# Performance work log

Measured on AMD Instinct MI355X. Metric: run time of the kernel, lower is better.

Reference implementation:

```python
import jax, jax.numpy as jnp
import numpy as np

N_NODES = 100000
N_EDGES = 1000000
H = 128  # hidden_size


def setup_inputs() -> dict:
    key = jax.random.key(0)
    ks = jax.random.split(key, 8)
    emb = jax.random.normal(ks[0], (N_NODES, H), dtype=jnp.float32)
    edge_index = jax.random.randint(ks[1], (2, N_EDGES), 0, N_NODES, dtype=jnp.int64)
    # MLP([2H, 4H, H, 1]) weights (Kaiming-ish scaled normals)
    W1 = jax.random.normal(ks[2], (2 * H, 4 * H), dtype=jnp.float32) / np.sqrt(2 * H).astype(np.float32)
    b1 = jnp.zeros((4 * H,), dtype=jnp.float32)
    W2 = jax.random.normal(ks[3], (4 * H, H), dtype=jnp.float32) / np.sqrt(4 * H).astype(np.float32)
    b2 = jnp.zeros((H,), dtype=jnp.float32)
    W3 = jax.random.normal(ks[4], (H, 1), dtype=jnp.float32) / np.sqrt(H).astype(np.float32)
    b3 = jnp.zeros((1,), dtype=jnp.float32)
    return {"emb": emb, "edge_index": edge_index,
            "W1": W1, "b1": b1, "W2": W2, "b2": b2, "W3": W3, "b3": b3}


def reference(emb, edge_index, W1, b1, W2, b2, W3, b3):
    # ExtractorMLP.forward with learn_edge_att=True, eval mode.
    col = edge_index[0]
    row = edge_index[1]
    # edge-gather + concat: [E, 2H]
    f12 = jnp.concatenate([emb[col], emb[row]], axis=-1)
    # MLP([2H, 4H, H, 1]); Dropout is identity in eval mode
    h = jax.nn.relu(f12 @ W1 + b1)          # [E, 4H]
    h = jax.nn.relu(h @ W2 + b2)            # [E, H]
    att_log_logits = h @ W3 + b3            # [E, 1]
    # concrete_sample with training=False -> plain sigmoid
    att = jax.nn.sigmoid(att_log_logits)
    return att
```

## Files before the change

kernel.cpp:

```cpp
#include <hip/hip_runtime.h>
#include <math.h>

#define E_TOTAL   1000000
#define HDIM      128
#define K1        256
#define N1        512
#define N2        128
#define M_TILE    64
#define BLOCK     512

typedef _Float16 f16;
typedef _Float16 f16_4 __attribute__((ext_vector_type(4)));
typedef _Float16 f16_8 __attribute__((ext_vector_type(8)));
typedef float    f32_4 __attribute__((ext_vector_type(4)));

__global__ void prep_kernel(const float* __restrict__ W1, const float* __restrict__ W2,
                            f16* __restrict__ W1F, f16* __restrict__ W2F) {
    int t = blockIdx.x * blockDim.x + threadIdx.x;
    const int total1 = K1 * N1;
    const int total2 = N1 * N2;
    if (t < total1) {
        int v    = t & 7;
        int lane = (t >> 3) & 63;
        int ks   = (t >> 9) & 7;
        int tile = t >> 12;
        int n = tile * 16 + (lane & 15);
        int k = ks * 32 + (lane >> 4) * 8 + v;
        W1F[t] = (f16)W1[k * N1 + n];
    } else if (t < total1 + total2) {
        int u = t - total1;
        int v    = u & 7;
        int lane = (u >> 3) & 63;
        int kc   = (u >> 9) & 15;
        int tile = u >> 13;
        int n = tile * 16 + (lane & 15);
        int k = kc * 32 + (lane >> 4) * 8 + v;
        W2F[u] = (f16)W2[k * N2 + n];
    }
}

__global__ __launch_bounds__(BLOCK, 4) void edge_mlp_kernel(
    const float* __restrict__ emb,
    const int*   __restrict__ eidx,
    const f16*   __restrict__ W1F,
    const float* __restrict__ b1,
    const f16*   __restrict__ W2F,
    const float* __restrict__ b2,
    const float* __restrict__ W3,
    const float* __restrict__ b3,
    float* __restrict__ out)
{
    __shared__ __align__(16) f16 sA[M_TILE * 256];
    __shared__ __align__(16) f16 sH1[M_TILE * 256];
    f16* sH2 = sA;

    const int tid = threadIdx.x;
    const int e0  = blockIdx.x * M_TILE;

    {
        const int m    = tid >> 3;
        const int side = (tid >> 2) & 1;
        const int sub  = tid & 3;
        const int node = eidx[side * E_TOTAL + e0 + m];
        const float4* src = (const float4*)(emb + (size_t)node * HDIM);
        #pragma unroll
        for (int i = 0; i < 8; ++i) {
            const int c4 = sub + 4 * i;
            float4 f = src[c4];
            f16_4 v = { (f16)f.x, (f16)f.y, (f16)f.z, (f16)f.w };
            const int ch  = side * 16 + (c4 >> 1);
            const int off = (c4 & 1) * 4;
            *(f16_4*)(sA + m * 256 + (((ch ^ (m & 7)) << 3) + off)) = v;
        }
    }
    __syncthreads();

    const int wv   = tid >> 6;
    const int lane = tid & 63;
    const int lrow = lane & 15;
    const int quad = lane >> 4;

    f32_4 acc2[4];
    #pragma unroll
    for (int et = 0; et < 4; ++et) acc2[et] = (f32_4){0.f, 0.f, 0.f, 0.f};

    #pragma unroll
    for (int h = 0; h < 2; ++h) {
        {
            f32_4 acc1[2][4];
            #pragma unroll
            for (int wnt = 0; wnt < 2; ++wnt)
                #pragma unroll
                for (int et = 0; et < 4; ++et) acc1[wnt][et] = (f32_4){0.f, 0.f, 0.f, 0.f};

            #pragma unroll
            for (int ks = 0; ks < 8; ++ks) {
                const int c = ks * 4 + quad;
                f16_8 ef[4];
                #pragma unroll
                for (int et = 0; et < 4; ++et) {
                    const int row = et * 16 + lrow;
                    ef[et] = *(const f16_8*)(sA + row * 256 + ((c ^ (row & 7)) << 3));
                }
                #pragma unroll
                for (int wnt = 0; wnt < 2; ++wnt) {
                    const int tile = h * 16 + wv * 2 + wnt;
                    f16_8 wf = *(const f16_8*)(W1F + (((tile * 8 + ks) * 64 + lane) << 3));
                    #pragma unroll
                    for (int et = 0; et < 4; ++et)
                        acc1[wnt][et] = __builtin_amdgcn_mfma_f32_16x16x32_f16(wf, ef[et], acc1[wnt][et], 0, 0, 0);
                }
            }
            #pragma unroll
            for (int wnt = 0; wnt < 2; ++wnt) {
                const float4 bias = *(const float4*)(b1 + h * 256 + wv * 32 + wnt * 16 + quad * 4);
                const int klocal = wv * 32 + wnt * 16 + quad * 4;
                const int ch  = klocal >> 3;
                const int off = klocal & 7;
                #pragma unroll
                for (int et = 0; et < 4; ++et) {
                    const int row = et * 16 + lrow;
                    f16_4 hv;
                    #pragma unroll
                    for (int i = 0; i < 4; ++i) {
                        float v = acc1[wnt][et][i] + ((const float*)&bias)[i];
                        hv[i] = (f16)(v > 0.f ? v : 0.f);
                    }
                    *(f16_4*)(sH1 + row * 256 + (((ch ^ (row & 7)) << 3) + off)) = hv;
                }
            }
        }
        __syncthreads();

        #pragma unroll
        for (int ks = 0; ks < 8; ++ks) {
            const int c = ks * 4 + quad;
            f16_8 ef[4];
            #pragma unroll
            for (int et = 0; et < 4; ++et) {
                const int row = et * 16 + lrow;
                ef[et] = *(const f16_8*)(sH1 + row * 256 + ((c ^ (row & 7)) << 3));
            }
            f16_8 wf = *(const f16_8*)(W2F + (((wv * 16 + h * 8 + ks) * 64 + lane) << 3));
            #pragma unroll
            for (int et = 0; et < 4; ++et)
                acc2[et] = __builtin_amdgcn_mfma_f32_16x16x32_f16(wf, ef[et], acc2[et], 0, 0, 0);
        }
        __syncthreads();
    }

    {
        const float4 b2v = *(const float4*)(b2 + wv * 16 + quad * 4);
        const int wn  = wv * 16 + quad * 4;
        const int ch  = wn >> 3;
        const int off = wn & 7;
        #pragma unroll
        for (int et = 0; et < 4; ++et) {
            const int row = et * 16 + lrow;
            f16_4 hv;
            #pragma unroll
            for (int i = 0; i < 4; ++i) {
                float v = acc2[et][i] + ((const float*)&b2v)[i];
                hv[i] = (f16)(v > 0.f ? v : 0.f);
            }
            *(f16_4*)(sH2 + row * 128 + (((ch ^ (row & 7)) << 3) + off)) = hv;
        }
    }
    __syncthreads();

    {
        const int m = tid >> 3;
        const int j = tid & 7;
        const int c0 = (2 * j)     ^ (m & 7);
        const int c1 = (2 * j + 1) ^ (m & 7);
        f16_8 a = *(const f16_8*)(sH2 + m * 128 + (c0 << 3));
        f16_8 b = *(const f16_8*)(sH2 + m * 128 + (c1 << 3));
        const float* w3p = W3 + j * 16;
        float s = 0.f;
        #pragma unroll
        for (int t = 0; t < 8; ++t) s += (float)a[t] * w3p[t];
        #pragma unroll
        for (int t = 0; t < 8; ++t) s += (float)b[t] * w3p[8 + t];
        s += __shfl_xor(s, 1);
        s += __shfl_xor(s, 2);
        s += __shfl_xor(s, 4);
        if (j == 0) {
            const float logit = s + b3[0];
            out[e0 + m] = 1.0f / (1.0f + __expf(-logit));
        }
    }
}

extern "C" void kernel_launch(void* const* d_in, const int* in_sizes, int n_in,
                              void* d_out, int out_size, void* d_ws, size_t ws_size,
                              hipStream_t stream) {
    const float* emb  = (const float*)d_in[0];
    const int*   eidx = (const int*)d_in[1];
    const float* W1   = (const float*)d_in[2];
    const float* b1   = (const float*)d_in[3];
    const float* W2   = (const float*)d_in[4];
    const float* b2   = (const float*)d_in[5];
    const float* W3   = (const float*)d_in[6];
    const float* b3   = (const float*)d_in[7];
    float* out = (float*)d_out;

    f16* W1F = (f16*)d_ws;
    f16* W2F = W1F + K1 * N1;

    const int prep_total = K1 * N1 + N1 * N2;
    prep_kernel<<<(prep_total + 255) / 256, 256, 0, stream>>>(W1, W2, W1F, W2F);

    edge_mlp_kernel<<<E_TOTAL / M_TILE, BLOCK, 0, stream>>>(
        emb, eidx, W1F, b1, W2F, b2, W3, b3, out);
}
```

Baseline: 688.4 us.

## Switch to 32x32x16 MFMA tiles and pre-convert embeddings to fp16

Replaces the 16x16x32 MFMA layout with 32x32x16 tiles. Each wave now owns one 32-row edge tile and two 32-column weight tiles, which cuts LDS A-fragment reads per MFMA, and both weight pre-pack layouts are rewritten to match. When the workspace is large enough, a separate pass converts the node embedding table to fp16, so the edge gather reads half the bytes per row. The cost is an extra conversion kernel (about 51 MB read, 26 MB written) and a workspace-size-dependent code path.

```diff
diff --git a/kernel.cpp b/kernel.cpp
--- a/kernel.cpp
+++ b/kernel.cpp
@@ -10,37 +10,46 @@
 #define BLOCK     512
 
 typedef _Float16 f16;
-typedef _Float16 f16_4 __attribute__((ext_vector_type(4)));
-typedef _Float16 f16_8 __attribute__((ext_vector_type(8)));
-typedef float    f32_4 __attribute__((ext_vector_type(4)));
-
-__global__ void prep_kernel(const float* __restrict__ W1, const float* __restrict__ W2,
-                            f16* __restrict__ W1F, f16* __restrict__ W2F) {
+typedef _Float16 f16_4  __attribute__((ext_vector_type(4)));
+typedef _Float16 f16_8  __attribute__((ext_vector_type(8)));
+typedef float    f32_16 __attribute__((ext_vector_type(16)));
+
+__global__ void prep_weights(const float* __restrict__ W1, const float* __restrict__ W2,
+                             f16* __restrict__ W1F, f16* __restrict__ W2F) {
     int t = blockIdx.x * blockDim.x + threadIdx.x;
     const int total1 = K1 * N1;
     const int total2 = N1 * N2;
     if (t < total1) {
         int v    = t & 7;
         int lane = (t >> 3) & 63;
-        int ks   = (t >> 9) & 7;
-        int tile = t >> 12;
-        int n = tile * 16 + (lane & 15);
-        int k = ks * 32 + (lane >> 4) * 8 + v;
+        int kc   = (t >> 9) & 15;
+        int nt   = t >> 13;
+        int k = kc * 16 + (lane >> 5) * 8 + v;
+        int n = nt * 32 + (lane & 31);
         W1F[t] = (f16)W1[k * N1 + n];
     } else if (t < total1 + total2) {
         int u = t - total1;
         int v    = u & 7;
         int lane = (u >> 3) & 63;
-        int kc   = (u >> 9) & 15;
-        int tile = u >> 13;
-        int n = tile * 16 + (lane & 15);
-        int k = kc * 32 + (lane >> 4) * 8 + v;
+        int kcg  = (u >> 9) & 31;
+        int nt   = u >> 14;
+        int k = kcg * 16 + (lane >> 5) * 8 + v;
+        int n = nt * 32 + (lane & 31);
         W2F[u] = (f16)W2[k * N2 + n];
     }
 }
 
+__global__ void prep_emb(const float* __restrict__ emb, f16* __restrict__ emb16) {
+    int t = blockIdx.x * blockDim.x + threadIdx.x;
+    float4 f = ((const float4*)emb)[t];
+    f16_4 v = { (f16)f.x, (f16)f.y, (f16)f.z, (f16)f.w };
+    ((f16_4*)emb16)[t] = v;
+}
+
+template <bool F16EMB>
 __global__ __launch_bounds__(BLOCK, 4) void edge_mlp_kernel(
     const float* __restrict__ emb,
+    const f16*   __restrict__ emb16,
     const int*   __restrict__ eidx,
     const f16*   __restrict__ W1F,
     const float* __restrict__ b1,
@@ -57,7 +66,20 @@
     const int tid = threadIdx.x;
     const int e0  = blockIdx.x * M_TILE;
 
-    {
+    if (F16EMB) {
+        const int row  = tid >> 2;
+        const int g    = tid & 3;
+        const int m    = row >> 1;
+        const int side = row & 1;
+        const int node = eidx[side * E_TOTAL + e0 + m];
+        const f16_8* src = (const f16_8*)(emb16 + (size_t)node * HDIM + g * 32);
+        #pragma unroll
+        for (int i = 0; i < 4; ++i) {
+            f16_8 v = src[i];
+            const int ch = side * 16 + g * 4 + i;
+            *(f16_8*)(sA + m * 256 + ((ch ^ (m & 7)) << 3)) = v;
+        }
+    } else {
         const int m    = tid >> 3;
         const int side = (tid >> 2) & 1;
         const int sub  = tid & 3;
@@ -77,93 +99,79 @@
 
     const int wv   = tid >> 6;
     const int lane = tid & 63;
-    const int lrow = lane & 15;
-    const int quad = lane >> 4;
-
-    f32_4 acc2[4];
+    const int l31  = lane & 31;
+    const int lh   = lane >> 5;
+    const int et   = wv & 1;
+    const int ntg  = wv >> 1;
+    const int arow = et * 32 + l31;
+    const int asw  = arow & 7;
+
+    f32_16 acc2 = {0.f};
+
     #pragma unroll
-    for (int et = 0; et < 4; ++et) acc2[et] = (f32_4){0.f, 0.f, 0.f, 0.f};
-
-    #pragma unroll
-    for (int h = 0; h < 2; ++h) {
+    for (int hh = 0; hh < 2; ++hh) {
         {
-            f32_4 acc1[2][4];
-            #pragma unroll
-            for (int wnt = 0; wnt < 2; ++wnt)
+            f32_16 acc1[2] = {{0.f}, {0.f}};
+            #pragma unroll
+            for (int kc = 0; kc < 16; ++kc) {
+                const int ch = kc * 2 + lh;
+                f16_8 ef = *(const f16_8*)(sA + arow * 256 + ((ch ^ asw) << 3));
                 #pragma unroll
-                for (int et = 0; et < 4; ++et) acc1[wnt][et] = (f32_4){0.f, 0.f, 0.f, 0.f};
-
-            #pragma unroll
-            for (int ks = 0; ks < 8; ++ks) {
-                const int c = ks * 4 + quad;
-                f16_8 ef[4];
+                for (int j = 0; j < 2; ++j) {
+                    const int nt = hh * 8 + ntg * 2 + j;
+                    f16_8 wf = *(const f16_8*)(W1F + (((nt * 16 + kc) * 64 + lane) << 3));
+                    acc1[j] = __builtin_amdgcn_mfma_f32_32x32x16_f16(wf, ef, acc1[j], 0, 0, 0);
+                }
+            }
+            #pragma unroll
+            for (int j = 0; j < 2; ++j) {
+                const int nth = ntg * 2 + j;
                 #pragma unroll
-                for (int et = 0; et < 4; ++et) {
-                    const int row = et * 16 + lrow;
-                    ef[et] = *(const f16_8*)(sA + row * 256 + ((c ^ (row & 7)) << 3));
-                }
-                #pragma unroll
-                for (int wnt = 0; wnt < 2; ++wnt) {
-                    const int tile = h * 16 + wv * 2 + wnt;
-                    f16_8 wf = *(const f16_8*)(W1F + (((tile * 8 + ks) * 64 + lane) << 3));
-                    #pragma unroll
-                    for (int et = 0; et < 4; ++et)
-                        acc1[wnt][et] = __builtin_amdgcn_mfma_f32_16x16x32_f16(wf, ef[et], acc1[wnt][et], 0, 0, 0);
-                }
-            }
-            #pragma unroll
-            for (int wnt = 0; wnt < 2; ++wnt) {
-                const float4 bias = *(const float4*)(b1 + h * 256 + wv * 32 + wnt * 16 + quad * 4);
-                const int klocal = wv * 32 + wnt * 16 + quad * 4;
-                const int ch  = klocal >> 3;
-                const int off = klocal & 7;
-                #pragma unroll
-                for (int et = 0; et < 4; ++et) {
-                    const int row = et * 16 + lrow;
+                for (int g = 0; g < 4; ++g) {
+                    const int wnh = nth * 32 + lh * 4 + g * 8;
+                    const float4 bv = *(const float4*)(b1 + hh * 256 + wnh);
                     f16_4 hv;
                     #pragma unroll
                     for (int i = 0; i < 4; ++i) {
-                        float v = acc1[wnt][et][i] + ((const float*)&bias)[i];
+                        float v = acc1[j][g * 4 + i] + ((const float*)&bv)[i];
                         hv[i] = (f16)(v > 0.f ? v : 0.f);
                     }
-                    *(f16_4*)(sH1 + row * 256 + (((ch ^ (row & 7)) << 3) + off)) = hv;
+                    const int ch  = wnh >> 3;
+                    const int off = wnh & 7;
+                    *(f16_4*)(sH1 + arow * 256 + (((ch ^ asw) << 3) + off)) = hv;
                 }
             }
         }
         __syncthreads();
 
+        {
+            const int nt2 = ntg;
+            #pragma unroll
+            for (int kc = 0; kc < 16; ++kc) {
+                const int ch = kc * 2 + lh;
+                f16_8 ef = *(const f16_8*)(sH1 + arow * 256 + ((ch ^ asw) << 3));
+                f16_8 wf = *(const f16_8*)(W2F + (((nt2 * 32 + hh * 16 + kc) * 64 + lane) << 3));
+                acc2 = __builtin_amdgcn_mfma_f32_32x32x16_f16(wf, ef, acc2, 0, 0, 0);
+            }
+        }
+        __syncthreads();
+    }
+
+    {
+        const int nt2 = ntg;
         #pragma unroll
-        for (int ks = 0; ks < 8; ++ks) {
-            const int c = ks * 4 + quad;
-            f16_8 ef[4];
-            #pragma unroll
-            for (int et = 0; et < 4; ++et) {
-                const int row = et * 16 + lrow;
-                ef[et] = *(const f16_8*)(sH1 + row * 256 + ((c ^ (row & 7)) << 3));
-            }
-            f16_8 wf = *(const f16_8*)(W2F + (((wv * 16 + h * 8 + ks) * 64 + lane) << 3));
-            #pragma unroll
-            for (int et = 0; et < 4; ++et)
-                acc2[et] = __builtin_amdgcn_mfma_f32_16x16x32_f16(wf, ef[et], acc2[et], 0, 0, 0);
-        }
-        __syncthreads();
-    }
-
-    {
-        const float4 b2v = *(const float4*)(b2 + wv * 16 + quad * 4);
-        const int wn  = wv * 16 + quad * 4;
-        const int ch  = wn >> 3;
-        const int off = wn & 7;
-        #pragma unroll
-        for (int et = 0; et < 4; ++et) {
-            const int row = et * 16 + lrow;
+        for (int g = 0; g < 4; ++g) {
+            const int wn = nt2 * 32 + lh * 4 + g * 8;
+            const float4 bv = *(const float4*)(b2 + wn);
             f16_4 hv;
             #pragma unroll
             for (int i = 0; i < 4; ++i) {
-                float v = acc2[et][i] + ((const float*)&b2v)[i];
+                float v = acc2[g * 4 + i] + ((const float*)&bv)[i];
                 hv[i] = (f16)(v > 0.f ? v : 0.f);
             }
-            *(f16_4*)(sH2 + row * 128 + (((ch ^ (row & 7)) << 3) + off)) = hv;
+            const int ch  = wn >> 3;
+            const int off = wn & 7;
+            *(f16_4*)(sH2 + arow * 128 + (((ch ^ asw) << 3) + off)) = hv;
         }
     }
     __syncthreads();
@@ -175,12 +183,13 @@
         const int c1 = (2 * j + 1) ^ (m & 7);
         f16_8 a = *(const f16_8*)(sH2 + m * 128 + (c0 << 3));
         f16_8 b = *(const f16_8*)(sH2 + m * 128 + (c1 << 3));
-        const float* w3p = W3 + j * 16;
+        const float4* w3v = (const float4*)(W3 + j * 16);
+        float4 w0 = w3v[0], w1 = w3v[1], w2 = w3v[2], w3 = w3v[3];
         float s = 0.f;
-        #pragma unroll
-        for (int t = 0; t < 8; ++t) s += (float)a[t] * w3p[t];
-        #pragma unroll
-        for (int t = 0; t < 8; ++t) s += (float)b[t] * w3p[8 + t];
+        s += (float)a[0]*w0.x + (float)a[1]*w0.y + (float)a[2]*w0.z + (float)a[3]*w0.w;
+        s += (float)a[4]*w1.x + (float)a[5]*w1.y + (float)a[6]*w1.z + (float)a[7]*w1.w;
+        s += (float)b[0]*w2.x + (float)b[1]*w2.y + (float)b[2]*w2.z + (float)b[3]*w2.w;
+        s += (float)b[4]*w3.x + (float)b[5]*w3.y + (float)b[6]*w3.z + (float)b[7]*w3.w;
         s += __shfl_xor(s, 1);
         s += __shfl_xor(s, 2);
         s += __shfl_xor(s, 4);
@@ -204,12 +213,23 @@
     const float* b3   = (const float*)d_in[7];
     float* out = (float*)d_out;
 
+    const size_t wbytes   = (size_t)(K1 * N1 + N1 * N2) * sizeof(f16);
+    const size_t embbytes = (size_t)100000 * HDIM * sizeof(f16);
+
     f16* W1F = (f16*)d_ws;
     f16* W2F = W1F + K1 * N1;
 
     const int prep_total = K1 * N1 + N1 * N2;
-    prep_kernel<<<(prep_total + 255) / 256, 256, 0, stream>>>(W1, W2, W1F, W2F);
-
-    edge_mlp_kernel<<<E_TOTAL / M_TILE, BLOCK, 0, stream>>>(
-        emb, eidx, W1F, b1, W2F, b2, W3, b3, out);
-}
+    prep_weights<<<(prep_total + 255) / 256, 256, 0, stream>>>(W1, W2, W1F, W2F);
+
+    if (ws_size >= wbytes + embbytes) {
+        f16* emb16 = W2F + N1 * N2;
+        const int cvt_threads = 100000 * HDIM / 4;
+        prep_emb<<<cvt_threads / 256, 256, 0, stream>>>(emb, emb16);
+        edge_mlp_kernel<true><<<E_TOTAL / M_TILE, BLOCK, 0, stream>>>(
+            emb, emb16, eidx, W1F, b1, W2F, b2, W3, b3, out);
+    } else {
+        edge_mlp_kernel<false><<<E_TOTAL / M_TILE, BLOCK, 0, stream>>>(
+            emb, (const f16*)nullptr, eidx, W1F, b1, W2F, b2, W3, b3, out);
+    }
+}
```

New measurement: 683.4 us. Within noise of the previous version (-0.7%).
